# Kernel optimization log

Hardware: AMD Instinct MI355X
Metric: run time of the kernel (lower is better)

## Reference

```python
import jax, jax.numpy as jnp
import numpy as np

D_MODEL = 2048
N_EXPERTS = 8
TOP_K = 2
FFN_HIDDEN = int(D_MODEL * 1.5)  # 3072, matches int(d_model*1.5)


def setup_inputs() -> dict:
    key = jax.random.key(0)
    k_x, k_r, k_g, k_u, k_d = jax.random.split(key, 5)
    B, L = 4, 4096
    s_in = 1.0 / np.sqrt(D_MODEL)
    s_hid = 1.0 / np.sqrt(FFN_HIDDEN)
    return {
        "x": jax.random.normal(k_x, (B, L, D_MODEL), dtype=jnp.float32),
        # nn.Linear weights are stored (out_features, in_features)
        "router_w": jax.random.uniform(k_r, (N_EXPERTS, D_MODEL), jnp.float32, -s_in, s_in),
        "gate_w": jax.random.uniform(k_g, (N_EXPERTS, FFN_HIDDEN, D_MODEL), jnp.float32, -s_in, s_in),
        "up_w": jax.random.uniform(k_u, (N_EXPERTS, FFN_HIDDEN, D_MODEL), jnp.float32, -s_in, s_in),
        "down_w": jax.random.uniform(k_d, (N_EXPERTS, D_MODEL, FFN_HIDDEN), jnp.float32, -s_hid, s_hid),
    }


def reference(x, router_w, gate_w, up_w, down_w):
    B, L, D = x.shape
    x_flat = x.reshape(-1, D)                                   # [N, D]

    router_logits = x_flat @ router_w.T                          # [N, E]
    router_probs = jax.nn.softmax(router_logits, axis=-1)
    top_k_probs, top_k_idx = jax.lax.top_k(router_probs, TOP_K)  # [N, K]
    top_k_probs = top_k_probs / jnp.sum(top_k_probs, axis=-1, keepdims=True)

    # combine[n, e] = sum_k top_k_probs[n,k] * (top_k_idx[n,k] == e)
    onehot = jax.nn.one_hot(top_k_idx, N_EXPERTS, dtype=x.dtype)  # [N, K, E]
    combine = jnp.einsum("nk,nke->ne", top_k_probs, onehot)       # [N, E]

    # Masked gather/scatter in the original == weight-0 tokens here; same math.
    output = jnp.zeros_like(x_flat)
    for e in range(N_EXPERTS):
        gate = jax.nn.silu(x_flat @ gate_w[e].T)                  # [N, H]
        up = x_flat @ up_w[e].T                                   # [N, H]
        expert_out = (gate * up) @ down_w[e].T                    # [N, D]
        output = output + combine[:, e:e + 1] * expert_out

    # dropout is identity in eval/reference mode
    return output.reshape(B, L, D)
```

## Files before the change

kernel.cpp:

```cpp
#include <hip/hip_runtime.h>
#include <hip/hip_bf16.h>
#include <cstdint>

#define N_TOK 16384
#define DMODEL 2048
#define FFH    3072
#define NGU    (2 * FFH)
#define NEXP   8
#define ATOT   32768

typedef __bf16 bf16;
typedef __attribute__((ext_vector_type(8))) __bf16 bf16x8;
typedef __attribute__((ext_vector_type(4))) __bf16 bf16x4;
typedef __attribute__((ext_vector_type(4))) float  f32x4;

__device__ __forceinline__ void gl_lds16(const bf16* g, void* l) {
  __builtin_amdgcn_global_load_lds(
      (const __attribute__((address_space(1))) void*)g,
      (__attribute__((address_space(3))) void*)l, 16, 0, 0);
}

__global__ void cvt_f32_bf16(const float* __restrict__ src, bf16* __restrict__ dst, long n4) {
  long i = (long)blockIdx.x * blockDim.x + threadIdx.x;
  if (i >= n4) return;
  const float4 v = ((const float4*)src)[i];
  bf16x4 o;
  o.x = (bf16)v.x; o.y = (bf16)v.y; o.z = (bf16)v.z; o.w = (bf16)v.w;
  ((bf16x4*)dst)[i] = o;
}

__global__ void cvt_guw(const float* __restrict__ gw, const float* __restrict__ uw,
                        bf16* __restrict__ guw) {
  const long i = (long)blockIdx.x * 256 + threadIdx.x;
  const int c8 = (int)(i & 255);
  const long rg = i >> 8;
  const int e = (int)(rg / NGU);
  const int ri = (int)(rg - (long)e * NGU);
  const int hb = ri >> 6, sub = ri & 63;
  const float* src = (sub < 32 ? gw : uw) + ((size_t)e * FFH + hb * 32 + (sub & 31)) * DMODEL + c8 * 8;
  const float4 v0 = ((const float4*)src)[0];
  const float4 v1 = ((const float4*)src)[1];
  bf16x8 o;
  o[0] = (bf16)v0.x; o[1] = (bf16)v0.y; o[2] = (bf16)v0.z; o[3] = (bf16)v0.w;
  o[4] = (bf16)v1.x; o[5] = (bf16)v1.y; o[6] = (bf16)v1.z; o[7] = (bf16)v1.w;
  *(bf16x8*)(guw + rg * DMODEL + c8 * 8) = o;
}

__global__ void router_k(const float* __restrict__ x, const float* __restrict__ rw,
                         int* __restrict__ tk_e, float* __restrict__ tk_w,
                         int* __restrict__ cnt) {
  const int wv = threadIdx.x >> 6, lane = threadIdx.x & 63;
  const int t = blockIdx.x * 4 + wv;
  const float* xr = x + (size_t)t * DMODEL;
  float acc[NEXP];
#pragma unroll
  for (int e = 0; e < NEXP; ++e) acc[e] = 0.f;
  for (int k = lane; k < DMODEL; k += 64) {
    const float xv = xr[k];
#pragma unroll
    for (int e = 0; e < NEXP; ++e) acc[e] = fmaf(xv, rw[e * DMODEL + k], acc[e]);
  }
#pragma unroll
  for (int e = 0; e < NEXP; ++e) {
#pragma unroll
    for (int o = 32; o; o >>= 1) acc[e] += __shfl_xor(acc[e], o, 64);
  }
  if (lane == 0) {
    int e0 = 0; float v0 = acc[0];
#pragma unroll
    for (int e = 1; e < NEXP; ++e) if (acc[e] > v0) { v0 = acc[e]; e0 = e; }
    int e1 = -1; float v1 = -1e30f;
#pragma unroll
    for (int e = 0; e < NEXP; ++e) if (e != e0 && acc[e] > v1) { v1 = acc[e]; e1 = e; }
    const float w0 = 1.f / (1.f + __expf(v1 - v0));
    tk_e[t * 2] = e0; tk_e[t * 2 + 1] = e1;
    tk_w[t * 2] = w0; tk_w[t * 2 + 1] = 1.f - w0;
    atomicAdd(&cnt[e0], 1); atomicAdd(&cnt[e1], 1);
  }
}

__global__ void offs_k(const int* __restrict__ cnt, int* __restrict__ offs) {
  if (threadIdx.x == 0) {
    int o = 0;
    for (int e = 0; e < NEXP; ++e) { offs[e] = o; o += cnt[e]; }
  }
}

__global__ void scatter_k(const int* __restrict__ tk_e, const float* __restrict__ tk_w,
                          const int* __restrict__ offs, int* __restrict__ cnt2,
                          int* __restrict__ tok_list, float* __restrict__ w_list,
                          int* __restrict__ aidx) {
  const int t = blockIdx.x * 256 + threadIdx.x;
  if (t >= N_TOK) return;
#pragma unroll
  for (int k = 0; k < 2; ++k) {
    const int e = tk_e[t * 2 + k];
    const int p = atomicAdd(&cnt2[e], 1);
    const int a = offs[e] + p;
    tok_list[a] = t;
    w_list[a] = tk_w[t * 2 + k];
    aidx[t * 2 + k] = a;
  }
}

template<int EPI>
__global__ __launch_bounds__(512, 2) void gemm_moe(
    const bf16* __restrict__ A, const bf16* __restrict__ B,
    bf16* __restrict__ hbuf, float* __restrict__ ybuf,
    const int* __restrict__ tok_list, const int* __restrict__ cnt,
    const int* __restrict__ offs) {
  constexpr int KD = EPI ? FFH : DMODEL;
  constexpr int NT = KD / 32;
  constexpr int BROWS = EPI ? DMODEL : NGU;

  const int e = blockIdx.z;
  const int cn = cnt[e];
  const int mbase = blockIdx.y * 256;
  if (mbase >= cn) return;
  const int offE = offs[e];
  const int nbase = blockIdx.x * 256;

  __shared__ char lds[98304];
  char* const ldsA = lds;
  char* const ldsB = lds + 49152;

  const int tid = threadIdx.x;
  const int wv = tid >> 6, lane = tid & 63;
  const int wr = wv >> 2, wc = wv & 3;

  const int sr = tid >> 2;
  const int swz8 = ((tid & 3) ^ ((tid >> 3) & 3)) * 8;
  const bf16* pA[2]; const bf16* pB[2];
  if (EPI == 0) {
    const int t0 = tok_list[offE + min(mbase + sr, cn - 1)];
    const int t1 = tok_list[offE + min(mbase + 128 + sr, cn - 1)];
    pA[0] = A + (size_t)t0 * KD + swz8;
    pA[1] = A + (size_t)t1 * KD + swz8;
  } else {
    const int a0 = offE + min(mbase + sr, cn - 1);
    const int a1 = offE + min(mbase + 128 + sr, cn - 1);
    pA[0] = A + (size_t)a0 * KD + swz8;
    pA[1] = A + (size_t)a1 * KD + swz8;
  }
  pB[0] = B + ((size_t)e * BROWS + nbase + sr) * KD + swz8;
  pB[1] = B + ((size_t)e * BROWS + nbase + 128 + sr) * KD + swz8;

  const int stageDst = wv * 1024;

  const int rswz = ((lane >> 4) ^ ((lane >> 1) & 3)) * 16;
  const int arow = (wr * 128 + (lane & 15)) * 64 + rswz;
  const int brow = (wc * 64 + (lane & 15)) * 64 + rswz;

  const f32x4 zero = {0.f, 0.f, 0.f, 0.f};
  f32x4 acc[8][4];
#pragma unroll
  for (int i = 0; i < 8; ++i)
#pragma unroll
    for (int j = 0; j < 4; ++j) acc[i][j] = zero;

  auto stage_half = [&](int buf, int q, int kt) {
    const int k8 = kt * 32;
    if (q < 2) gl_lds16(pA[q] + k8, ldsA + buf * 16384 + q * 8192 + stageDst);
    else       gl_lds16(pB[q - 2] + k8, ldsB + buf * 16384 + (q - 2) * 8192 + stageDst);
  };

#pragma unroll
  for (int q = 0; q < 4; ++q) stage_half(0, q, 0);
#pragma unroll
  for (int q = 0; q < 4; ++q) stage_half(1, q, 1);
  asm volatile("s_waitcnt vmcnt(4)" ::: "memory");
  __builtin_amdgcn_s_barrier();
  asm volatile("" ::: "memory");

  int cb = 0;
  for (int kt = 0; kt < NT; ++kt) {
    const int sb = (cb + 2 >= 3) ? cb - 1 : cb + 2;
    const char* cA = ldsA + cb * 16384;
    const char* cB = ldsB + cb * 16384;

    bf16x8 a[8], b[4];
#pragma unroll
    for (int i = 0; i < 4; ++i) {
      a[i] = *(const bf16x8*)(cA + i * 1024 + arow);
      b[i] = *(const bf16x8*)(cB + i * 1024 + brow);
    }
#pragma unroll
    for (int i = 4; i < 8; ++i) a[i] = *(const bf16x8*)(cA + i * 1024 + arow);

    if (kt + 2 < NT) { stage_half(sb, 0, kt + 2); stage_half(sb, 1, kt + 2); }

    __builtin_amdgcn_s_setprio(1);
#pragma unroll
    for (int nf = 0; nf < 4; ++nf)
#pragma unroll
      for (int mi = 0; mi < 4; ++mi)
        acc[mi][nf] = __builtin_amdgcn_mfma_f32_16x16x32_bf16(a[mi], b[nf], acc[mi][nf], 0, 0, 0);
    __builtin_amdgcn_s_setprio(0);

    if (kt + 2 < NT) { stage_half(sb, 2, kt + 2); stage_half(sb, 3, kt + 2); }

    __builtin_amdgcn_s_setprio(1);
#pragma unroll
    for (int nf = 0; nf < 4; ++nf)
#pragma unroll
      for (int mi = 4; mi < 8; ++mi)
        acc[mi][nf] = __builtin_amdgcn_mfma_f32_16x16x32_bf16(a[mi], b[nf], acc[mi][nf], 0, 0, 0);
    __builtin_amdgcn_s_setprio(0);

    if (kt + 2 < NT) { asm volatile("s_waitcnt vmcnt(4)" ::: "memory"); }
    else             { asm volatile("s_waitcnt vmcnt(0)" ::: "memory"); }
    asm volatile("" ::: "memory");
    __builtin_amdgcn_s_barrier();
    asm volatile("" ::: "memory");

    cb = (cb + 1 == 3) ? 0 : cb + 1;
  }

  const int col = lane & 15;
  const int rb = mbase + wr * 128 + (lane >> 4) * 4;
  if (EPI == 0) {
    const int hb32 = ((nbase + wc * 64) >> 6) * 32;
#pragma unroll
    for (int mi = 0; mi < 8; ++mi)
#pragma unroll
      for (int j = 0; j < 4; ++j) {
        const int row = rb + mi * 16 + j;
        if (row < cn) {
          bf16* hr = hbuf + (size_t)(offE + row) * FFH + hb32 + col;
#pragma unroll
          for (int k = 0; k < 2; ++k) {
            const float g = acc[mi][k][j], u = acc[mi][k + 2][j];
            hr[k * 16] = (bf16)(g / (1.f + __expf(-g)) * u);
          }
        }
      }
  } else {
#pragma unroll
    for (int mi = 0; mi < 8; ++mi)
#pragma unroll
      for (int j = 0; j < 4; ++j) {
        const int row = rb + mi * 16 + j;
        if (row < cn) {
          float* yr = ybuf + (size_t)(offE + row) * DMODEL + nbase + wc * 64 + col;
#pragma unroll
          for (int nf = 0; nf < 4; ++nf) yr[nf * 16] = acc[mi][nf][j];
        }
      }
  }
}

__global__ void combine_k(const float* __restrict__ ybuf, const int* __restrict__ aidx,
                          const float* __restrict__ tk_w, float* __restrict__ out) {
  const int i = blockIdx.x * 256 + threadIdx.x;
  const int t = i >> 9, c = i & 511;
  const int a0 = aidx[t * 2], a1 = aidx[t * 2 + 1];
  const float w0 = tk_w[t * 2], w1 = tk_w[t * 2 + 1];
  const float4 v0 = ((const float4*)(ybuf + (size_t)a0 * DMODEL))[c];
  const float4 v1 = ((const float4*)(ybuf + (size_t)a1 * DMODEL))[c];
  float4 o;
  o.x = w0 * v0.x + w1 * v1.x;
  o.y = w0 * v0.y + w1 * v1.y;
  o.z = w0 * v0.z + w1 * v1.z;
  o.w = w0 * v0.w + w1 * v1.w;
  ((float4*)(out + (size_t)t * DMODEL))[c] = o;
}

extern "C" void kernel_launch(void* const* d_in, const int* in_sizes, int n_in,
                              void* d_out, int out_size, void* d_ws, size_t ws_size,
                              hipStream_t stream) {
  const float* x  = (const float*)d_in[0];
  const float* rw = (const float*)d_in[1];
  const float* gw = (const float*)d_in[2];
  const float* uw = (const float*)d_in[3];
  const float* dw = (const float*)d_in[4];
  float* out = (float*)d_out;

  char* ws = (char*)d_ws;
  size_t o = 0;
  auto alloc = [&](size_t bytes) {
    void* p = ws + o;
    o = (o + bytes + 255) & ~(size_t)255;
    return p;
  };

  const size_t guw_bytes  = (size_t)NEXP * NGU * DMODEL * 2;
  const size_t ybuf_bytes = (size_t)(ATOT + 256) * DMODEL * 4;
  bf16*  xb       = (bf16*)alloc((size_t)N_TOK * DMODEL * 2);
  void*  uni      = alloc(ybuf_bytes > guw_bytes ? ybuf_bytes : guw_bytes);
  bf16*  guw      = (bf16*)uni;
  float* ybuf     = (float*)uni;
  bf16*  dwb      = (bf16*)alloc((size_t)NEXP * DMODEL * FFH * 2);
  bf16*  hbuf     = (bf16*)alloc((size_t)(ATOT + 256) * FFH * 2);
  int*   tok_list = (int*)alloc((ATOT + 256) * 4);
  float* w_list   = (float*)alloc((ATOT + 256) * 4);
  int*   tk_e     = (int*)alloc((size_t)N_TOK * 2 * 4);
  float* tk_w     = (float*)alloc((size_t)N_TOK * 2 * 4);
  int*   aidx     = (int*)alloc((size_t)N_TOK * 2 * 4);
  int*   cnt      = (int*)alloc(64);
  int*   offs     = (int*)alloc(64);
  int*   cnt2     = (int*)alloc(64);

  hipMemsetAsync(cnt, 0, 64, stream);
  hipMemsetAsync(cnt2, 0, 64, stream);

  {
    long n4 = (long)N_TOK * DMODEL / 4;
    cvt_f32_bf16<<<(unsigned)(n4 / 256), 256, 0, stream>>>(x, xb, n4);
  }
  cvt_guw<<<(unsigned)((long)NEXP * NGU * DMODEL / 8 / 256), 256, 0, stream>>>(gw, uw, guw);
  {
    long n4 = (long)NEXP * DMODEL * FFH / 4;
    cvt_f32_bf16<<<(unsigned)(n4 / 256), 256, 0, stream>>>(dw, dwb, n4);
  }

  router_k<<<N_TOK / 4, 256, 0, stream>>>(x, rw, tk_e, tk_w, cnt);
  offs_k<<<1, 64, 0, stream>>>(cnt, offs);
  scatter_k<<<N_TOK / 256, 256, 0, stream>>>(tk_e, tk_w, offs, cnt2, tok_list, w_list, aidx);

  gemm_moe<0><<<dim3(NGU / 256, 64, NEXP), 512, 0, stream>>>(
      xb, guw, hbuf, nullptr, tok_list, cnt, offs);
  gemm_moe<1><<<dim3(DMODEL / 256, 64, NEXP), 512, 0, stream>>>(
      hbuf, dwb, nullptr, ybuf, tok_list, cnt, offs);

  combine_k<<<N_TOK * 512 / 256, 256, 0, stream>>>(ybuf, aidx, tk_w, out);
}
```

Measured before the change: 1.999 ms.

## Restructure MoE GEMM main loop to double-buffered 64-wide K tiles

After: 2.023 ms. About the same (+1.2%).

```diff
diff --git a/kernel.cpp b/kernel.cpp
--- a/kernel.cpp
+++ b/kernel.cpp
@@ -110,7 +110,7 @@
     const int* __restrict__ tok_list, const int* __restrict__ cnt,
     const int* __restrict__ offs) {
   constexpr int KD = EPI ? FFH : DMODEL;
-  constexpr int NT = KD / 32;
+  constexpr int NT = KD / 64;
   constexpr int BROWS = EPI ? DMODEL : NGU;
 
   const int e = blockIdx.z;
@@ -120,9 +120,9 @@
   const int offE = offs[e];
   const int nbase = blockIdx.x * 256;
 
-  __shared__ char lds[98304];
+  __shared__ char lds[131072];
   char* const ldsA = lds;
-  char* const ldsB = lds + 49152;
+  char* const ldsB = lds + 65536;
 
   const int tid = threadIdx.x;
   const int wv = tid >> 6, lane = tid & 63;
@@ -145,11 +145,11 @@
   pB[0] = B + ((size_t)e * BROWS + nbase + sr) * KD + swz8;
   pB[1] = B + ((size_t)e * BROWS + nbase + 128 + sr) * KD + swz8;
 
-  const int stageDst = wv * 1024;
+  const int stageDst = (tid >> 2) * 64 + (tid & 3) * 16;
 
   const int rswz = ((lane >> 4) ^ ((lane >> 1) & 3)) * 16;
-  const int arow = (wr * 128 + (lane & 15)) * 64 + rswz;
-  const int brow = (wc * 64 + (lane & 15)) * 64 + rswz;
+  const int aoff = (wr * 128 + (lane & 15)) * 64 + rswz;
+  const int boff = (wc * 64 + (lane & 15)) * 64 + rswz;
 
   const f32x4 zero = {0.f, 0.f, 0.f, 0.f};
   f32x4 acc[8][4];
@@ -158,62 +158,75 @@
 #pragma unroll
     for (int j = 0; j < 4; ++j) acc[i][j] = zero;
 
-  auto stage_half = [&](int buf, int q, int kt) {
-    const int k8 = kt * 32;
-    if (q < 2) gl_lds16(pA[q] + k8, ldsA + buf * 16384 + q * 8192 + stageDst);
-    else       gl_lds16(pB[q - 2] + k8, ldsB + buf * 16384 + (q - 2) * 8192 + stageDst);
+  auto stageA = [&](int d, int kh, int kt) {
+    char* dst = ldsA + d * 32768 + kh * 16384 + stageDst;
+    const int ko = kt * 64 + kh * 32;
+    gl_lds16(pA[0] + ko, dst);
+    gl_lds16(pA[1] + ko, dst + 8192);
   };
-
-#pragma unroll
-  for (int q = 0; q < 4; ++q) stage_half(0, q, 0);
-#pragma unroll
-  for (int q = 0; q < 4; ++q) stage_half(1, q, 1);
+  auto stageB = [&](int d, int kh, int kt) {
+    char* dst = ldsB + d * 32768 + kh * 16384 + stageDst;
+    const int ko = kt * 64 + kh * 32;
+    gl_lds16(pB[0] + ko, dst);
+    gl_lds16(pB[1] + ko, dst + 8192);
+  };
+
+  stageA(0, 0, 0); stageB(0, 0, 0); stageA(0, 1, 0); stageB(0, 1, 0);
   asm volatile("s_waitcnt vmcnt(4)" ::: "memory");
   __builtin_amdgcn_s_barrier();
   asm volatile("" ::: "memory");
 
-  int cb = 0;
+  int dbf = 0;
   for (int kt = 0; kt < NT; ++kt) {
-    const int sb = (cb + 2 >= 3) ? cb - 1 : cb + 2;
-    const char* cA = ldsA + cb * 16384;
-    const char* cB = ldsB + cb * 16384;
-
-    bf16x8 a[8], b[4];
-#pragma unroll
-    for (int i = 0; i < 4; ++i) {
-      a[i] = *(const bf16x8*)(cA + i * 1024 + arow);
-      b[i] = *(const bf16x8*)(cB + i * 1024 + brow);
+    const bool pf = (kt + 1 < NT);
+#pragma unroll
+    for (int kh = 0; kh < 2; ++kh) {
+      const char* Ak = ldsA + dbf * 32768 + kh * 16384;
+      const char* Bk = ldsB + dbf * 32768 + kh * 16384;
+
+      bf16x8 a[4], b[4];
+#pragma unroll
+      for (int i = 0; i < 4; ++i) {
+        a[i] = *(const bf16x8*)(Ak + i * 1024 + aoff);
+        b[i] = *(const bf16x8*)(Bk + i * 1024 + boff);
+      }
+      if (pf) stageA(dbf ^ 1, kh, kt + 1);
+      asm volatile("" ::: "memory");
+      __builtin_amdgcn_s_barrier();
+      asm volatile("" ::: "memory");
+      __builtin_amdgcn_s_setprio(1);
+#pragma unroll
+      for (int nf = 0; nf < 4; ++nf)
+#pragma unroll
+        for (int i = 0; i < 4; ++i)
+          acc[i][nf] = __builtin_amdgcn_mfma_f32_16x16x32_bf16(a[i], b[nf], acc[i][nf], 0, 0, 0);
+      __builtin_amdgcn_s_setprio(0);
+      asm volatile("" ::: "memory");
+      __builtin_amdgcn_s_barrier();
+      asm volatile("" ::: "memory");
+
+      bf16x8 a2[4];
+#pragma unroll
+      for (int i = 0; i < 4; ++i)
+        a2[i] = *(const bf16x8*)(Ak + (4 + i) * 1024 + aoff);
+      if (pf) stageB(dbf ^ 1, kh, kt + 1);
+      asm volatile("" ::: "memory");
+      __builtin_amdgcn_s_barrier();
+      asm volatile("" ::: "memory");
+      __builtin_amdgcn_s_setprio(1);
+#pragma unroll
+      for (int nf = 0; nf < 4; ++nf)
+#pragma unroll
+        for (int i = 0; i < 4; ++i)
+          acc[4 + i][nf] = __builtin_amdgcn_mfma_f32_16x16x32_bf16(a2[i], b[nf], acc[4 + i][nf], 0, 0, 0);
+      __builtin_amdgcn_s_setprio(0);
+      if (pf) { asm volatile("s_waitcnt vmcnt(4)" ::: "memory"); }
+      else    { asm volatile("s_waitcnt vmcnt(0)" ::: "memory"); }
+      asm volatile("" ::: "memory");
+      __builtin_amdgcn_s_barrier();
+      asm volatile("" ::: "memory");
     }
-#pragma unroll
-    for (int i = 4; i < 8; ++i) a[i] = *(const bf16x8*)(cA + i * 1024 + arow);
-
-    if (kt + 2 < NT) { stage_half(sb, 0, kt + 2); stage_half(sb, 1, kt + 2); }
-
-    __builtin_amdgcn_s_setprio(1);
-#pragma unroll
-    for (int nf = 0; nf < 4; ++nf)
-#pragma unroll
-      for (int mi = 0; mi < 4; ++mi)
-        acc[mi][nf] = __builtin_amdgcn_mfma_f32_16x16x32_bf16(a[mi], b[nf], acc[mi][nf], 0, 0, 0);
-    __builtin_amdgcn_s_setprio(0);
-
-    if (kt + 2 < NT) { stage_half(sb, 2, kt + 2); stage_half(sb, 3, kt + 2); }
-
-    __builtin_amdgcn_s_setprio(1);
-#pragma unroll
-    for (int nf = 0; nf < 4; ++nf)
-#pragma unroll
-      for (int mi = 4; mi < 8; ++mi)
-        acc[mi][nf] = __builtin_amdgcn_mfma_f32_16x16x32_bf16(a[mi], b[nf], acc[mi][nf], 0, 0, 0);
-    __builtin_amdgcn_s_setprio(0);
-
-    if (kt + 2 < NT) { asm volatile("s_waitcnt vmcnt(4)" ::: "memory"); }
-    else             { asm volatile("s_waitcnt vmcnt(0)" ::: "memory"); }
-    asm volatile("" ::: "memory");
-    __builtin_amdgcn_s_barrier();
-    asm volatile("" ::: "memory");
-
-    cb = (cb + 1 == 3) ? 0 : cb + 1;
+    dbf ^= 1;
   }
 
   const int col = lane & 15;
```
